# Kernel tuning notes

Hardware: AMD Instinct MI355X
Metric: run time of the kernel (lower is better)

Reference implementation:

```python
import jax, jax.numpy as jnp
import numpy as np

NEG_INF = -1e9


def _gru_cell(x, h, W_ih, W_hh, b_ih, b_hh):
    # torch GRUCell math, gate order [r; z; n]
    gx = x @ W_ih.T + b_ih          # [B, 3H]
    gh = h @ W_hh.T + b_hh          # [B, 3H]
    xr, xz, xn = jnp.split(gx, 3, axis=-1)
    hr, hz, hn = jnp.split(gh, 3, axis=-1)
    r = jax.nn.sigmoid(xr + hr)
    z = jax.nn.sigmoid(xz + hz)
    n = jnp.tanh(xn + r * hn)
    return (1.0 - z) * n + z * h


def setup_inputs() -> dict:
    key = jax.random.key(0)
    ks = jax.random.split(key, 8)
    B, N, D, H, P = 64, 2048, 256, 256, 256
    s = 0.05
    return {
        "sequence": jax.random.normal(ks[0], (B, N, D), jnp.float32),
        "hidden_t": jax.random.normal(ks[1], (B, H), jnp.float32),
        "sequence_mask": jnp.ones((B, N), jnp.float32),
        "num_steps": 2,
        "W_seq": jax.random.normal(ks[2], (D, P), jnp.float32) * s,
        "W_h": jax.random.normal(ks[3], (H, P), jnp.float32) * s,
        "v_att": jax.random.normal(ks[4], (P,), jnp.float32) * s,
        "W_ih": jax.random.normal(ks[5], (3 * H, D), jnp.float32) * s,
        "W_hh": jax.random.normal(ks[6], (3 * H, H), jnp.float32) * s,
        "b_ih": jnp.zeros((3 * H,), jnp.float32),
        "b_hh": jnp.zeros((3 * H,), jnp.float32),
    }


def reference(sequence, hidden_t, sequence_mask, num_steps,
              W_seq, W_h, v_att, W_ih, W_hh, b_ih, b_hh):
    # Precompute the sequence projection once (invariant across decode steps).
    seq_proj = jnp.einsum("bnd,dp->bnp", sequence, W_seq)   # [B, N, P]
    mask_bias = jnp.where(sequence_mask > 0, 0.0, NEG_INF)  # [B, N]

    def step(h, _):
        # projection similarity: v . tanh(W1 s_i + W2 h)
        proj = jnp.tanh(seq_proj + (h @ W_h)[:, None, :])   # [B, N, P]
        scores = jnp.einsum("bnp,p->bn", proj, v_att) + mask_bias
        w = jax.nn.softmax(scores, axis=-1)                  # [B, N]
        vec = jnp.einsum("bn,bnd->bd", w, sequence)          # [B, D]
        h_new = _gru_cell(vec, h, W_ih, W_hh, b_ih, b_hh)
        return h_new, w

    _, ws = jax.lax.scan(step, hidden_t, None, length=num_steps)  # [T, B, N]
    return jnp.transpose(ws, (1, 0, 2))                            # [B, T, N]
```

## Files before the change

kernel.cpp:

```cpp
#include <hip/hip_runtime.h>
#include <cstdint>

using u16 = unsigned short;
using u32 = unsigned int;
typedef __attribute__((ext_vector_type(8))) short bf16x8;
typedef __attribute__((ext_vector_type(8))) u16 u16x8;
typedef __attribute__((ext_vector_type(16))) float f32x16;
typedef __attribute__((ext_vector_type(4))) u16 u16x4;
typedef __attribute__((ext_vector_type(4))) u32 u32x4;

#define DEV static __device__ __forceinline__

DEV u16 bf16_rne(float x) {
  u32 u = __float_as_uint(x);
  u32 r = (u + 0x7FFFu + ((u >> 16) & 1u)) >> 16;
  return (u16)r;
}
DEV float bf16f(u16 h) { return __uint_as_float(((u32)h) << 16); }

DEV u32 cvt_pk_bf16(float lo, float hi) {
  u32 d;
  asm("v_cvt_pk_bf16_f32 %0, %1, %2" : "=v"(d) : "v"(lo), "v"(hi));
  return d;
}

DEV float fast_tanh(float x) {
  float e = __expf(2.0f * x);
  return 1.0f - 2.0f / (e + 1.0f);
}
DEV float sigmoidf_(float x) { return 1.0f / (1.0f + __expf(-x)); }

__global__ __launch_bounds__(256) void prep_w(const float* __restrict__ Wseq,
                                              const float* __restrict__ Wih,
                                              const float* __restrict__ Whh,
                                              u16* __restrict__ WfG,
                                              float* __restrict__ WT,
                                              float* __restrict__ UT) {
  const int bid = blockIdx.x, t = threadIdx.x;
  if (bid < 32) {
    const int unit = bid * 4 + (t >> 6);
    const int lane = t & 63, l31 = lane & 31, koct = lane >> 5;
    const int pt8 = unit >> 4, kt = unit & 15;
    u16x8 o;
#pragma unroll
    for (int e = 0; e < 8; ++e)
      o[e] = bf16_rne(
          Wseq[(long)(kt * 16 + koct * 8 + e) * 256 + pt8 * 32 + l31]);
    *(u16x8*)(WfG + (long)unit * 512 + lane * 8) = o;
  } else {
    const int gid = bid - 32;
    const float* src = (gid >= 12) ? Whh : Wih;
    float* dst = (gid >= 12) ? UT : WT;
    const int g = (gid % 12) * 64 + (t & 63);
    const int dq = t >> 6;
#pragma unroll 4
    for (int d = dq * 64; d < dq * 64 + 64; ++d)
      dst[(long)d * 768 + g] = src[(long)g * 256 + d];
  }
}

template <int STEP0>
__global__ __launch_bounds__(1024) void bigstep(
    const float* __restrict__ seq, u16* __restrict__ seqF,
    const u16* __restrict__ WfG, const float* __restrict__ hprev,
    const float* __restrict__ Wh, const float* __restrict__ vatt,
    const float* __restrict__ mask, float* __restrict__ wbuf,
    float* __restrict__ esum, float* __restrict__ part, int N, int NCH,
    int B) {
  __shared__ u16 sR[65536];
  __shared__ float sQ[256][5];
  __shared__ float se[256], shw[256], svv[256], sredE[4];
  __shared__ float sHW[4][256];

  const int t = threadIdx.x, lane = t & 63, w = t >> 6;
  const int l31 = lane & 31, koct = lane >> 5;
  const int pg = w >> 2, ng = w & 3;
  const int b = blockIdx.y, cpair = blockIdx.x;
  char* sRb = (char*)sR;

  auto fillChunk = [&](int chunk) {
    if constexpr (STEP0) {
      const float* src = seq + ((long)b * N + chunk * 256) * 256;
#pragma unroll
      for (int i = 0; i < 8; ++i) {
        const int idx = i * 8192 + t * 8;
        float4 x = *(const float4*)(src + idx);
        float4 y = *(const float4*)(src + idx + 4);
        u32x4 o;
        o[0] = cvt_pk_bf16(x.x, x.y);
        o[1] = cvt_pk_bf16(x.z, x.w);
        o[2] = cvt_pk_bf16(y.x, y.y);
        o[3] = cvt_pk_bf16(y.z, y.w);
        const int row = idx >> 8, colb = (idx & 255) * 2;
        *(u32x4*)(sRb + row * 512 + (colb ^ ((row & 31) << 4))) = o;
      }
    } else {
      const u16* src = seqF + ((long)(b * NCH + chunk) << 16);
#pragma unroll
      for (int i = 0; i < 8; ++i) {
        const u16* g = src + ((long)(i * 1024 + t)) * 8;
        char* l = sRb + ((size_t)(i * 1024 + (t & ~63)) * 16);
        __builtin_amdgcn_global_load_lds(
            (const __attribute__((address_space(1))) u32*)g,
            (__attribute__((address_space(3))) u32*)l, 16, 0, 0);
      }
    }
  };

  auto writeoutChunk = [&](int chunk) {
    u16* dst = seqF + ((long)(b * NCH + chunk) << 16);
#pragma unroll
    for (int i = 0; i < 8; ++i) {
      const int u = i * 1024 + t;
      const int ln = u & 63, kt = (u >> 6) & 15, t8 = u >> 10;
      const int row = t8 * 32 + (ln & 31);
      const int colb = (kt * 16 + (ln >> 5) * 8) * 2;
      u16x8 v = *(const u16x8*)(sRb + row * 512 + (colb ^ ((row & 31) << 4)));
      *(u16x8*)(dst + (long)u * 8) = v;
    }
  };

  auto gemmChunk = [&](f32x16& a00, f32x16& a01, f32x16& a10, f32x16& a11) {
    const u16* wa0 = WfG + (long)(pg * 32) * 512 + lane * 8;
    const u16* wa1 = wa0 + 16 * 512;
    const char* p0;
    const char* p1;
    int sw0 = 0, sw1 = 0, cb = 0;
    if constexpr (STEP0) {
      const int row0 = ng * 64 + l31, row1 = row0 + 32;
      p0 = sRb + row0 * 512;
      p1 = sRb + row1 * 512;
      sw0 = (row0 & 31) << 4;
      sw1 = (row1 & 31) << 4;
      cb = koct * 16;
    } else {
      p0 = sRb + (size_t)(ng * 32768) + lane * 16;
      p1 = p0 + 16384;
    }
#pragma unroll 4
    for (int kt = 0; kt < 16; ++kt) {
      bf16x8 af0 = *(const bf16x8*)(wa0 + kt * 512);
      bf16x8 af1 = *(const bf16x8*)(wa1 + kt * 512);
      bf16x8 bf0, bf1;
      if constexpr (STEP0) {
        bf0 = *(const bf16x8*)(p0 + ((kt * 32 + cb) ^ sw0));
        bf1 = *(const bf16x8*)(p1 + ((kt * 32 + cb) ^ sw1));
      } else {
        bf0 = *(const bf16x8*)(p0 + kt * 1024);
        bf1 = *(const bf16x8*)(p1 + kt * 1024);
      }
      a00 = __builtin_amdgcn_mfma_f32_32x32x16_bf16(af0, bf0, a00, 0, 0, 0);
      a01 = __builtin_amdgcn_mfma_f32_32x32x16_bf16(af0, bf1, a01, 0, 0, 0);
      a10 = __builtin_amdgcn_mfma_f32_32x32x16_bf16(af1, bf0, a10, 0, 0, 0);
      a11 = __builtin_amdgcn_mfma_f32_32x32x16_bf16(af1, bf1, a11, 0, 0, 0);
    }
  };

  auto epiChunk = [&](int chunk, const f32x16& a00, const f32x16& a01,
                      const f32x16& a10, const f32x16& a11) {
    float sc0 = 0.f, sc1 = 0.f;
#pragma unroll
    for (int r = 0; r < 16; ++r) {
      const int pidx = pg * 64 + (r & 3) + 8 * (r >> 2) + 4 * koct;
      const float pv = svv[pidx], ph = shw[pidx];
      sc0 = fmaf(pv, fast_tanh(a00[r] + ph), sc0);
      sc1 = fmaf(pv, fast_tanh(a01[r] + ph), sc1);
    }
#pragma unroll
    for (int r = 0; r < 16; ++r) {
      const int pidx = pg * 64 + 32 + (r & 3) + 8 * (r >> 2) + 4 * koct;
      const float pv = svv[pidx], ph = shw[pidx];
      sc0 = fmaf(pv, fast_tanh(a10[r] + ph), sc0);
      sc1 = fmaf(pv, fast_tanh(a11[r] + ph), sc1);
    }
    sc0 += __shfl_xor(sc0, 32, 64);
    sc1 += __shfl_xor(sc1, 32, 64);
    if (koct == 0) {
      sQ[ng * 64 + l31][pg] = sc0;
      sQ[ng * 64 + 32 + l31][pg] = sc1;
    }
    __syncthreads();
    if (t < 256) {
      float s = (sQ[t][0] + sQ[t][1]) + (sQ[t][2] + sQ[t][3]);
      const long n = (long)b * N + chunk * 256 + t;
      float e = (mask[n] > 0.f) ? __expf(s) : 0.f;
      se[t] = e;
      wbuf[n] = e;
      float s4 = e;
#pragma unroll
      for (int off = 1; off < 64; off <<= 1) s4 += __shfl_xor(s4, off, 64);
      if ((t & 63) == 0) sredE[t >> 6] = s4;
    }
    __syncthreads();
    if (t == 0)
      esum[b * NCH + chunk] = (sredE[0] + sredE[1]) + (sredE[2] + sredE[3]);
    const u16* bs = seqF + ((long)(b * NCH + chunk) << 16);
    const int kt = w;
    float vd0 = 0, vd1 = 0, vd2 = 0, vd3 = 0, vd4 = 0, vd5 = 0, vd6 = 0,
          vd7 = 0;
    const u16* vb = bs + ((long)kt * 64 + lane) * 8;
#pragma unroll
    for (int t8 = 0; t8 < 8; ++t8) {
      u16x8 q = *(const u16x8*)(vb + (long)t8 * 8192);
      const float wv = se[t8 * 32 + l31];
      vd0 = fmaf(wv, bf16f((u16)q[0]), vd0);
      vd1 = fmaf(wv, bf16f((u16)q[1]), vd1);
      vd2 = fmaf(wv, bf16f((u16)q[2]), vd2);
      vd3 = fmaf(wv, bf16f((u16)q[3]), vd3);
      vd4 = fmaf(wv, bf16f((u16)q[4]), vd4);
      vd5 = fmaf(wv, bf16f((u16)q[5]), vd5);
      vd6 = fmaf(wv, bf16f((u16)q[6]), vd6);
      vd7 = fmaf(wv, bf16f((u16)q[7]), vd7);
    }
#pragma unroll
    for (int off = 1; off < 32; off <<= 1) {
      vd0 += __shfl_xor(vd0, off, 64);
      vd1 += __shfl_xor(vd1, off, 64);
      vd2 += __shfl_xor(vd2, off, 64);
      vd3 += __shfl_xor(vd3, off, 64);
      vd4 += __shfl_xor(vd4, off, 64);
      vd5 += __shfl_xor(vd5, off, 64);
      vd6 += __shfl_xor(vd6, off, 64);
      vd7 += __shfl_xor(vd7, off, 64);
    }
    if (l31 == 0) {
      float4 o0 = {vd0, vd1, vd2, vd3};
      float4 o1 = {vd4, vd5, vd6, vd7};
      float* pp = part + (long)(chunk * B + b) * 256 + kt * 16 + koct * 8;
      *(float4*)pp = o0;
      *(float4*)(pp + 4) = o1;
    }
  };

  const int c0 = cpair * 2, c1 = c0 + 1;
  fillChunk(c0);
  {
    const int p_ = t & 255, kq = t >> 8;
    const float* hp = hprev + b * 256 + kq * 64;
    const float* whp = Wh + (long)kq * 64 * 256 + p_;
    float hacc = 0.f;
#pragma unroll 8
    for (int k = 0; k < 64; ++k) hacc = fmaf(hp[k], whp[(long)k * 256], hacc);
    sHW[kq][p_] = hacc;
    if (t < 256) svv[t] = vatt[t];
  }
  __syncthreads();
  if (t < 256) shw[t] = (sHW[0][t] + sHW[1][t]) + (sHW[2][t] + sHW[3][t]);
  if constexpr (STEP0) writeoutChunk(c0);
  f32x16 a00 = (f32x16)0.f, a01 = (f32x16)0.f, a10 = (f32x16)0.f,
         a11 = (f32x16)0.f;
  gemmChunk(a00, a01, a10, a11);
  __syncthreads();
  fillChunk(c1);
  epiChunk(c0, a00, a01, a10, a11);
  if constexpr (STEP0) writeoutChunk(c1);
  f32x16 b00 = (f32x16)0.f, b01 = (f32x16)0.f, b10 = (f32x16)0.f,
         b11 = (f32x16)0.f;
  gemmChunk(b00, b01, b10, b11);
  epiChunk(c1, b00, b01, b10, b11);
}

__global__ __launch_bounds__(256) void finalize_gru(
    const float* __restrict__ part, const float* __restrict__ esumP, int ecnt,
    const float* __restrict__ hprev, const float* __restrict__ WT,
    const float* __restrict__ UT, const float* __restrict__ bih,
    const float* __restrict__ bhh, const float* __restrict__ wbuf,
    float* __restrict__ out, float* __restrict__ hnew, int N, int T, int step,
    int NP, int B) {
  const int q = blockIdx.x, b = blockIdx.y, t = threadIdx.x;
  __shared__ float sv[256], sh[256], sP[6][4][64];
  float S = 0.f;
  for (int i = 0; i < ecnt; ++i) S += esumP[b * ecnt + i];
  const float inv = 1.f / S;
  float a = 0.f;
  for (int cc = 0; cc < NP; ++cc) a += part[((long)cc * B + b) * 256 + t];
  sv[t] = a * inv;
  sh[t] = hprev[b * 256 + t];
  __syncthreads();
  const int j4 = t & 63, dg = t >> 6;
  const int j = q * 64 + j4;
  float g0 = 0, g1 = 0, g2 = 0, g3 = 0, g4 = 0, g5 = 0;
#pragma unroll 4
  for (int d = dg * 64; d < dg * 64 + 64; ++d) {
    const float vd = sv[d], hd = sh[d];
    const float* wr_ = WT + (long)d * 768 + j;
    const float* ur_ = UT + (long)d * 768 + j;
    g0 = fmaf(vd, wr_[0], g0);
    g1 = fmaf(vd, wr_[256], g1);
    g2 = fmaf(vd, wr_[512], g2);
    g3 = fmaf(hd, ur_[0], g3);
    g4 = fmaf(hd, ur_[256], g4);
    g5 = fmaf(hd, ur_[512], g5);
  }
  sP[0][dg][j4] = g0;
  sP[1][dg][j4] = g1;
  sP[2][dg][j4] = g2;
  sP[3][dg][j4] = g3;
  sP[4][dg][j4] = g4;
  sP[5][dg][j4] = g5;
  __syncthreads();
  if (t < 64) {
    const int jj = q * 64 + t;
    float xr = bih[jj], xz = bih[256 + jj], xn = bih[512 + jj];
    float hr = bhh[jj], hz = bhh[256 + jj], hn = bhh[512 + jj];
#pragma unroll
    for (int dgg = 0; dgg < 4; ++dgg) {
      xr += sP[0][dgg][t];
      xz += sP[1][dgg][t];
      xn += sP[2][dgg][t];
      hr += sP[3][dgg][t];
      hz += sP[4][dgg][t];
      hn += sP[5][dgg][t];
    }
    float rr = sigmoidf_(xr + hr);
    float zz = sigmoidf_(xz + hz);
    float nn = fast_tanh(xn + rr * hn);
    hnew[b * 256 + jj] = (1.f - zz) * nn + zz * sh[jj];
  }
  const long ob = ((long)b * T + step) * N;
  const int nq = N >> 2;
  for (int i = 0; i * 256 < nq; ++i) {
    const int n = q * nq + i * 256 + t;
    out[ob + n] = wbuf[(long)b * N + n] * inv;
  }
}

extern "C" void kernel_launch(void* const* d_in, const int* in_sizes, int n_in,
                              void* d_out, int out_size, void* d_ws,
                              size_t ws_size, hipStream_t stream) {
  (void)n_in;
  (void)ws_size;
  const float* seq = (const float*)d_in[0];
  const float* hidden = (const float*)d_in[1];
  const float* mask = (const float*)d_in[2];
  const float* Wseq = (const float*)d_in[4];
  const float* Wh = (const float*)d_in[5];
  const float* vatt = (const float*)d_in[6];
  const float* Wih = (const float*)d_in[7];
  const float* Whh = (const float*)d_in[8];
  const float* bih = (const float*)d_in[9];
  const float* bhh = (const float*)d_in[10];
  float* out = (float*)d_out;

  const int P = in_sizes[6];
  const int H = in_sizes[5] / P;
  const int B = in_sizes[1] / H;
  const int N = in_sizes[2] / B;
  const int T = out_size / (B * N);
  const long M = (long)B * N;
  const int NCH = N / 256;

  char* p = (char*)d_ws;
  auto alloc = [&](size_t bytes) {
    char* r = p;
    p += (bytes + 255) & ~(size_t)255;
    return r;
  };
  u16* seqF = (u16*)alloc((size_t)M * 256 * 2);
  u16* WfG = (u16*)alloc((size_t)256 * 256 * 2);
  float* WT = (float*)alloc((size_t)256 * 768 * 4);
  float* UT = (float*)alloc((size_t)256 * 768 * 4);
  float* wbuf = (float*)alloc((size_t)B * N * 4);
  float* hA = (float*)alloc((size_t)B * 256 * 4);
  float* hB = (float*)alloc((size_t)B * 256 * 4);
  float* part = (float*)alloc((size_t)NCH * B * 256 * 4);
  float* esum = (float*)alloc((size_t)B * NCH * 4);
  float* hbuf[2] = {hA, hB};

  prep_w<<<dim3(56), dim3(256), 0, stream>>>(Wseq, Wih, Whh, WfG, WT, UT);

  for (int t = 0; t < T; ++t) {
    const float* hcur = (t == 0) ? hidden : hbuf[(t - 1) & 1];
    if (t == 0) {
      bigstep<1><<<dim3(NCH / 2, B), dim3(1024), 0, stream>>>(
          seq, seqF, WfG, hcur, Wh, vatt, mask, wbuf, esum, part, N, NCH, B);
    } else {
      bigstep<0><<<dim3(NCH / 2, B), dim3(1024), 0, stream>>>(
          seq, seqF, WfG, hcur, Wh, vatt, mask, wbuf, esum, part, N, NCH, B);
    }
    finalize_gru<<<dim3(4, B), dim3(256), 0, stream>>>(
        part, esum, NCH, hcur, WT, UT, bih, bhh, wbuf, out, hbuf[t & 1], N, T,
        t, NCH, B);
  }
}
```

Before: 161.5 us.

## Shrink bigstep blocks to 128-row chunks with 512 threads for higher occupancy

Each bigstep block now handles one 128-row chunk with 512 threads and 64KB LDS, replacing a 1024-thread block that processed two 256-row chunks back to back with a software-pipelined prefetch. The intent is to get more resident blocks per CU (launch bounds 512,4) and more blocks overall, so memory latency is hidden by occupancy rather than by manual overlap. The h·W_h projection is now computed by 256 threads over the full K instead of being split four ways. Costs: that hW projection is recomputed by twice as many blocks, there are twice as many partial sums for finalize_gru to reduce, and the explicit fill/compute overlap is gone.

After: 177.4 us. +9.8%, slower.

```diff
diff --git a/kernel.cpp b/kernel.cpp
--- a/kernel.cpp
+++ b/kernel.cpp
@@ -60,67 +60,77 @@
 }
 
 template <int STEP0>
-__global__ __launch_bounds__(1024) void bigstep(
+__global__ __launch_bounds__(512, 4) void bigstep(
     const float* __restrict__ seq, u16* __restrict__ seqF,
     const u16* __restrict__ WfG, const float* __restrict__ hprev,
     const float* __restrict__ Wh, const float* __restrict__ vatt,
     const float* __restrict__ mask, float* __restrict__ wbuf,
-    float* __restrict__ esum, float* __restrict__ part, int N, int NCH,
+    float* __restrict__ esum, float* __restrict__ part, int N, int NCH2,
     int B) {
-  __shared__ u16 sR[65536];
-  __shared__ float sQ[256][5];
-  __shared__ float se[256], shw[256], svv[256], sredE[4];
-  __shared__ float sHW[4][256];
+  __shared__ __align__(16) u16 sR[32768];
+  __shared__ float sQ[128][5];
+  __shared__ float se[128], shw[256], svv[256], sredE[2];
 
   const int t = threadIdx.x, lane = t & 63, w = t >> 6;
   const int l31 = lane & 31, koct = lane >> 5;
-  const int pg = w >> 2, ng = w & 3;
-  const int b = blockIdx.y, cpair = blockIdx.x;
+  const int pg = w >> 1, ng = w & 1;
+  const int b = blockIdx.y, ch = blockIdx.x;
   char* sRb = (char*)sR;
-
-  auto fillChunk = [&](int chunk) {
-    if constexpr (STEP0) {
-      const float* src = seq + ((long)b * N + chunk * 256) * 256;
-#pragma unroll
-      for (int i = 0; i < 8; ++i) {
-        const int idx = i * 8192 + t * 8;
-        float4 x = *(const float4*)(src + idx);
-        float4 y = *(const float4*)(src + idx + 4);
-        u32x4 o;
-        o[0] = cvt_pk_bf16(x.x, x.y);
-        o[1] = cvt_pk_bf16(x.z, x.w);
-        o[2] = cvt_pk_bf16(y.x, y.y);
-        o[3] = cvt_pk_bf16(y.z, y.w);
-        const int row = idx >> 8, colb = (idx & 255) * 2;
-        *(u32x4*)(sRb + row * 512 + (colb ^ ((row & 31) << 4))) = o;
-      }
-    } else {
-      const u16* src = seqF + ((long)(b * NCH + chunk) << 16);
-#pragma unroll
-      for (int i = 0; i < 8; ++i) {
-        const u16* g = src + ((long)(i * 1024 + t)) * 8;
-        char* l = sRb + ((size_t)(i * 1024 + (t & ~63)) * 16);
-        __builtin_amdgcn_global_load_lds(
-            (const __attribute__((address_space(1))) u32*)g,
-            (__attribute__((address_space(3))) u32*)l, 16, 0, 0);
-      }
-    }
-  };
-
-  auto writeoutChunk = [&](int chunk) {
-    u16* dst = seqF + ((long)(b * NCH + chunk) << 16);
+  const long chbase = (long)(b * NCH2 + ch) << 15;
+
+  if constexpr (STEP0) {
+    const float* src = seq + ((long)b * N + ch * 128) * 256;
 #pragma unroll
     for (int i = 0; i < 8; ++i) {
-      const int u = i * 1024 + t;
-      const int ln = u & 63, kt = (u >> 6) & 15, t8 = u >> 10;
+      const int idx = i * 4096 + t * 8;
+      float4 x = *(const float4*)(src + idx);
+      float4 y = *(const float4*)(src + idx + 4);
+      u32x4 o;
+      o[0] = cvt_pk_bf16(x.x, x.y);
+      o[1] = cvt_pk_bf16(x.z, x.w);
+      o[2] = cvt_pk_bf16(y.x, y.y);
+      o[3] = cvt_pk_bf16(y.z, y.w);
+      const int row = idx >> 8, colb = (idx & 255) * 2;
+      *(u32x4*)(sRb + row * 512 + (colb ^ ((row & 31) << 4))) = o;
+    }
+  } else {
+    const u16* src = seqF + chbase;
+#pragma unroll
+    for (int i = 0; i < 8; ++i) {
+      const u16* g = src + ((long)(i * 512 + t)) * 8;
+      char* l = sRb + ((size_t)(i * 512 + (t & ~63)) * 16);
+      __builtin_amdgcn_global_load_lds(
+          (const __attribute__((address_space(1))) u32*)g,
+          (__attribute__((address_space(3))) u32*)l, 16, 0, 0);
+    }
+  }
+  if (t < 256) {
+    const float* hp = hprev + b * 256;
+    float hacc = 0.f;
+#pragma unroll 8
+    for (int k = 0; k < 256; ++k) hacc = fmaf(hp[k], Wh[(long)k * 256 + t], hacc);
+    shw[t] = hacc;
+    svv[t] = vatt[t];
+  }
+  __syncthreads();
+
+  if constexpr (STEP0) {
+    u16* dst = seqF + chbase;
+#pragma unroll
+    for (int i = 0; i < 8; ++i) {
+      const int uidx = i * 512 + t;
+      const int ln = uidx & 63, unit = uidx >> 6;
+      const int kt = unit & 15, t8 = unit >> 4;
       const int row = t8 * 32 + (ln & 31);
       const int colb = (kt * 16 + (ln >> 5) * 8) * 2;
       u16x8 v = *(const u16x8*)(sRb + row * 512 + (colb ^ ((row & 31) << 4)));
-      *(u16x8*)(dst + (long)u * 8) = v;
-    }
-  };
-
-  auto gemmChunk = [&](f32x16& a00, f32x16& a01, f32x16& a10, f32x16& a11) {
+      *(u16x8*)(dst + (long)uidx * 8) = v;
+    }
+  }
+
+  f32x16 a00 = (f32x16)0.f, a01 = (f32x16)0.f, a10 = (f32x16)0.f,
+         a11 = (f32x16)0.f;
+  {
     const u16* wa0 = WfG + (long)(pg * 32) * 512 + lane * 8;
     const u16* wa1 = wa0 + 16 * 512;
     const char* p0;
@@ -154,54 +164,53 @@
       a10 = __builtin_amdgcn_mfma_f32_32x32x16_bf16(af1, bf0, a10, 0, 0, 0);
       a11 = __builtin_amdgcn_mfma_f32_32x32x16_bf16(af1, bf1, a11, 0, 0, 0);
     }
-  };
-
-  auto epiChunk = [&](int chunk, const f32x16& a00, const f32x16& a01,
-                      const f32x16& a10, const f32x16& a11) {
-    float sc0 = 0.f, sc1 = 0.f;
-#pragma unroll
-    for (int r = 0; r < 16; ++r) {
-      const int pidx = pg * 64 + (r & 3) + 8 * (r >> 2) + 4 * koct;
-      const float pv = svv[pidx], ph = shw[pidx];
-      sc0 = fmaf(pv, fast_tanh(a00[r] + ph), sc0);
-      sc1 = fmaf(pv, fast_tanh(a01[r] + ph), sc1);
-    }
-#pragma unroll
-    for (int r = 0; r < 16; ++r) {
-      const int pidx = pg * 64 + 32 + (r & 3) + 8 * (r >> 2) + 4 * koct;
-      const float pv = svv[pidx], ph = shw[pidx];
-      sc0 = fmaf(pv, fast_tanh(a10[r] + ph), sc0);
-      sc1 = fmaf(pv, fast_tanh(a11[r] + ph), sc1);
-    }
-    sc0 += __shfl_xor(sc0, 32, 64);
-    sc1 += __shfl_xor(sc1, 32, 64);
-    if (koct == 0) {
-      sQ[ng * 64 + l31][pg] = sc0;
-      sQ[ng * 64 + 32 + l31][pg] = sc1;
-    }
-    __syncthreads();
-    if (t < 256) {
-      float s = (sQ[t][0] + sQ[t][1]) + (sQ[t][2] + sQ[t][3]);
-      const long n = (long)b * N + chunk * 256 + t;
-      float e = (mask[n] > 0.f) ? __expf(s) : 0.f;
-      se[t] = e;
-      wbuf[n] = e;
-      float s4 = e;
-#pragma unroll
-      for (int off = 1; off < 64; off <<= 1) s4 += __shfl_xor(s4, off, 64);
-      if ((t & 63) == 0) sredE[t >> 6] = s4;
-    }
-    __syncthreads();
-    if (t == 0)
-      esum[b * NCH + chunk] = (sredE[0] + sredE[1]) + (sredE[2] + sredE[3]);
-    const u16* bs = seqF + ((long)(b * NCH + chunk) << 16);
-    const int kt = w;
+  }
+
+  float sc0 = 0.f, sc1 = 0.f;
+#pragma unroll
+  for (int r = 0; r < 16; ++r) {
+    const int pidx = pg * 64 + (r & 3) + 8 * (r >> 2) + 4 * koct;
+    const float pv = svv[pidx], ph = shw[pidx];
+    sc0 = fmaf(pv, fast_tanh(a00[r] + ph), sc0);
+    sc1 = fmaf(pv, fast_tanh(a01[r] + ph), sc1);
+  }
+#pragma unroll
+  for (int r = 0; r < 16; ++r) {
+    const int pidx = pg * 64 + 32 + (r & 3) + 8 * (r >> 2) + 4 * koct;
+    const float pv = svv[pidx], ph = shw[pidx];
+    sc0 = fmaf(pv, fast_tanh(a10[r] + ph), sc0);
+    sc1 = fmaf(pv, fast_tanh(a11[r] + ph), sc1);
+  }
+  sc0 += __shfl_xor(sc0, 32, 64);
+  sc1 += __shfl_xor(sc1, 32, 64);
+  if (koct == 0) {
+    sQ[ng * 64 + l31][pg] = sc0;
+    sQ[ng * 64 + 32 + l31][pg] = sc1;
+  }
+  __syncthreads();
+  if (t < 128) {
+    float s = (sQ[t][0] + sQ[t][1]) + (sQ[t][2] + sQ[t][3]);
+    const long n = (long)b * N + ch * 128 + t;
+    float e = (mask[n] > 0.f) ? __expf(s) : 0.f;
+    se[t] = e;
+    wbuf[n] = e;
+    float s4 = e;
+#pragma unroll
+    for (int off = 1; off < 64; off <<= 1) s4 += __shfl_xor(s4, off, 64);
+    if ((t & 63) == 0) sredE[t >> 6] = s4;
+  }
+  __syncthreads();
+  if (t == 0) esum[b * NCH2 + ch] = sredE[0] + sredE[1];
+
+  const u16* bs = seqF + chbase;
+#pragma unroll
+  for (int kk = 0; kk < 2; ++kk) {
+    const int kt = w + kk * 8;
     float vd0 = 0, vd1 = 0, vd2 = 0, vd3 = 0, vd4 = 0, vd5 = 0, vd6 = 0,
           vd7 = 0;
-    const u16* vb = bs + ((long)kt * 64 + lane) * 8;
-#pragma unroll
-    for (int t8 = 0; t8 < 8; ++t8) {
-      u16x8 q = *(const u16x8*)(vb + (long)t8 * 8192);
+#pragma unroll
+    for (int t8 = 0; t8 < 4; ++t8) {
+      u16x8 q = *(const u16x8*)(bs + ((long)(t8 * 16 + kt) * 64 + lane) * 8);
       const float wv = se[t8 * 32 + l31];
       vd0 = fmaf(wv, bf16f((u16)q[0]), vd0);
       vd1 = fmaf(wv, bf16f((u16)q[1]), vd1);
@@ -226,38 +235,11 @@
     if (l31 == 0) {
       float4 o0 = {vd0, vd1, vd2, vd3};
       float4 o1 = {vd4, vd5, vd6, vd7};
-      float* pp = part + (long)(chunk * B + b) * 256 + kt * 16 + koct * 8;
+      float* pp = part + (long)(ch * B + b) * 256 + kt * 16 + koct * 8;
       *(float4*)pp = o0;
       *(float4*)(pp + 4) = o1;
     }
-  };
-
-  const int c0 = cpair * 2, c1 = c0 + 1;
-  fillChunk(c0);
-  {
-    const int p_ = t & 255, kq = t >> 8;
-    const float* hp = hprev + b * 256 + kq * 64;
-    const float* whp = Wh + (long)kq * 64 * 256 + p_;
-    float hacc = 0.f;
-#pragma unroll 8
-    for (int k = 0; k < 64; ++k) hacc = fmaf(hp[k], whp[(long)k * 256], hacc);
-    sHW[kq][p_] = hacc;
-    if (t < 256) svv[t] = vatt[t];
-  }
-  __syncthreads();
-  if (t < 256) shw[t] = (sHW[0][t] + sHW[1][t]) + (sHW[2][t] + sHW[3][t]);
-  if constexpr (STEP0) writeoutChunk(c0);
-  f32x16 a00 = (f32x16)0.f, a01 = (f32x16)0.f, a10 = (f32x16)0.f,
-         a11 = (f32x16)0.f;
-  gemmChunk(a00, a01, a10, a11);
-  __syncthreads();
-  fillChunk(c1);
-  epiChunk(c0, a00, a01, a10, a11);
-  if constexpr (STEP0) writeoutChunk(c1);
-  f32x16 b00 = (f32x16)0.f, b01 = (f32x16)0.f, b10 = (f32x16)0.f,
-         b11 = (f32x16)0.f;
-  gemmChunk(b00, b01, b10, b11);
-  epiChunk(c1, b00, b01, b10, b11);
+  }
 }
 
 __global__ __launch_bounds__(256) void finalize_gru(
@@ -348,7 +330,7 @@
   const int N = in_sizes[2] / B;
   const int T = out_size / (B * N);
   const long M = (long)B * N;
-  const int NCH = N / 256;
+  const int NCH2 = N / 128;
 
   char* p = (char*)d_ws;
   auto alloc = [&](size_t bytes) {
@@ -363,8 +345,8 @@
   float* wbuf = (float*)alloc((size_t)B * N * 4);
   float* hA = (float*)alloc((size_t)B * 256 * 4);
   float* hB = (float*)alloc((size_t)B * 256 * 4);
-  float* part = (float*)alloc((size_t)NCH * B * 256 * 4);
-  float* esum = (float*)alloc((size_t)B * NCH * 4);
+  float* part = (float*)alloc((size_t)NCH2 * B * 256 * 4);
+  float* esum = (float*)alloc((size_t)B * NCH2 * 4);
   float* hbuf[2] = {hA, hB};
 
   prep_w<<<dim3(56), dim3(256), 0, stream>>>(Wseq, Wih, Whh, WfG, WT, UT);
@@ -372,14 +354,14 @@
   for (int t = 0; t < T; ++t) {
     const float* hcur = (t == 0) ? hidden : hbuf[(t - 1) & 1];
     if (t == 0) {
-      bigstep<1><<<dim3(NCH / 2, B), dim3(1024), 0, stream>>>(
-          seq, seqF, WfG, hcur, Wh, vatt, mask, wbuf, esum, part, N, NCH, B);
+      bigstep<1><<<dim3(NCH2, B), dim3(512), 0, stream>>>(
+          seq, seqF, WfG, hcur, Wh, vatt, mask, wbuf, esum, part, N, NCH2, B);
     } else {
-      bigstep<0><<<dim3(NCH / 2, B), dim3(1024), 0, stream>>>(
-          seq, seqF, WfG, hcur, Wh, vatt, mask, wbuf, esum, part, N, NCH, B);
+      bigstep<0><<<dim3(NCH2, B), dim3(512), 0, stream>>>(
+          seq, seqF, WfG, hcur, Wh, vatt, mask, wbuf, esum, part, N, NCH2, B);
     }
     finalize_gru<<<dim3(4, B), dim3(256), 0, stream>>>(
-        part, esum, NCH, hcur, WT, UT, bih, bhh, wbuf, out, hbuf[t & 1], N, T,
-        t, NCH, B);
-  }
-}
+        part, esum, NCH2, hcur, WT, UT, bih, bhh, wbuf, out, hbuf[t & 1], N, T,
+        t, NCH2, B);
+  }
+}
```
